# Performance work log

Measured on AMD Instinct MI355X. Metric: run time of the kernel, lower is better.

## Reference

```python
import jax, jax.numpy as jnp
import numpy as np


def setup_inputs() -> dict:
    key = jax.random.key(0)
    ks = jax.random.split(key, 6)
    B, C, W, H = 8, 512, 64, 64
    return {
        "x": jax.random.normal(ks[0], (B, C, W, H), dtype=jnp.float32),
        "proj_query": jax.random.normal(ks[1], (C, W, H), dtype=jnp.float32),
        "key_w": jax.random.normal(ks[2], (C, C), dtype=jnp.float32) * 0.02,
        "key_b": jax.random.normal(ks[3], (C,), dtype=jnp.float32) * 0.02,
        "value_w": jax.random.normal(ks[4], (C, C), dtype=jnp.float32) * 0.02,
        "value_b": jax.random.normal(ks[5], (C,), dtype=jnp.float32) * 0.02,
        "gamma": jnp.ones((1,), dtype=jnp.float32),
    }


def reference(x, proj_query, key_w, key_b, value_w, value_b, gamma):
    B, C, W, H = x.shape
    N = W * H
    # fixed memory query: (C, N); torch builds B x N x C via permute
    q = proj_query.reshape(C, N)
    # 1x1 convs == per-pixel channel matmuls
    k = jnp.einsum('oc,bchw->bohw', key_w, x) + key_b[None, :, None, None]
    v = jnp.einsum('oc,bchw->bohw', value_w, x) + value_b[None, :, None, None]
    k = k.reshape(B, C, N)
    v = v.reshape(B, C, N)
    # energy = bmm(key [B,C,N], query^T [N,C]) -> B x C x C (channel attention)
    energy = jnp.einsum('bcn,dn->bcd', k, q)
    attention = jax.nn.softmax(energy, axis=-1)
    # out = bmm(attention^T [B,C,C], value [B,C,N]) -> B x C x N
    out = jnp.einsum('bdc,bdn->bcn', attention, v)
    out = out.reshape(B, C, W, H)
    return gamma * out + x
```

## Files before the change

### kernel.cpp

```cpp
#include <hip/hip_runtime.h>

typedef unsigned short u16;
typedef unsigned int u32;
typedef unsigned long long u64;
typedef _Float16 f16x8 __attribute__((ext_vector_type(8)));
typedef float f32x4 __attribute__((ext_vector_type(4)));

__device__ __forceinline__ u16 f2h(float f) {
  union { _Float16 h; u16 u; } c; c.h = (_Float16)f; return c.u;
}
__device__ __forceinline__ float h2f(u16 v) {
  union { u16 u; _Float16 h; } c; c.u = v; return (float)c.h;
}

__device__ __forceinline__ f32x4 mfma16(f16x8 a, f16x8 b, f32x4 c) {
  return __builtin_amdgcn_mfma_f32_16x16x32_f16(a, b, c, 0, 0, 0);
}

__device__ __forceinline__ void ld8f(const float* s, u16* o) {
  float4 a = *(const float4*)s;
  float4 b = *(const float4*)(s + 4);
  o[0] = f2h(a.x); o[1] = f2h(a.y); o[2] = f2h(a.z); o[3] = f2h(a.w);
  o[4] = f2h(b.x); o[5] = f2h(b.y); o[6] = f2h(b.z); o[7] = f2h(b.w);
}

__device__ __forceinline__ void cvt8(float4 a, float4 b, u16* o) {
  o[0] = f2h(a.x); o[1] = f2h(a.y); o[2] = f2h(a.z); o[3] = f2h(a.w);
  o[4] = f2h(b.x); o[5] = f2h(b.y); o[6] = f2h(b.z); o[7] = f2h(b.w);
}

__device__ __forceinline__ void addcvt8(float4 a0, float4 a1, float4 c0, float4 c1, u16* o) {
  o[0] = f2h(a0.x + c0.x); o[1] = f2h(a0.y + c0.y); o[2] = f2h(a0.z + c0.z); o[3] = f2h(a0.w + c0.w);
  o[4] = f2h(a1.x + c1.x); o[5] = f2h(a1.y + c1.y); o[6] = f2h(a1.z + c1.z); o[7] = f2h(a1.w + c1.w);
}

__device__ __forceinline__ void glds16(const u16* g, u16* l) {
  __builtin_amdgcn_global_load_lds(
      reinterpret_cast<const __attribute__((address_space(1))) u32*>(reinterpret_cast<u64>(g)),
      reinterpret_cast<__attribute__((address_space(3))) u32*>(reinterpret_cast<u64>(l)),
      16, 0, 0);
}

template<int TM, int TN, int WM, int WN, int DEPTH>
__device__ __forceinline__ void gemm_core(const u16* __restrict__ A, int lda,
                                          const u16* __restrict__ B, int ldb,
                                          int ksteps, u16* sA, u16* sB, f32x4 acc[TM][TN]) {
  constexpr int NT = WM * WN * 64;
  constexpr int BM = WM * TM * 16, BN = WN * TN * 16;
  constexpr int TILEA = BM * 32, TILEB = BN * 32;
  constexpr int APF = (BM * 4) / NT, BPF = (BN * 4) / NT;
  constexpr int VPI = APF + BPF;
  constexpr int PF = DEPTH - 2;
  static_assert(PF == 1 || PF == 2, "");
  static_assert(APF >= 1 && BPF >= 1, "");

  const int t = threadIdx.x;
  const int lane = t & 63, wave = t >> 6;
  const int wm = wave / WN, wn = wave % WN;
  const int m16 = lane & 15, q4 = lane >> 4;

  int aoff[APF], asl[APF];
#pragma unroll
  for (int p = 0; p < APF; ++p) {
    int s = p * NT + t, row = s >> 2;
    int kc = (s & 3) ^ ((row >> 1) & 3);
    aoff[p] = row * lda + kc * 8;
    asl[p] = (p * NT + (wave << 6)) * 8;
  }
  int boff[BPF], bsl[BPF];
#pragma unroll
  for (int p = 0; p < BPF; ++p) {
    int s = p * NT + t, row = s >> 2;
    int kc = (s & 3) ^ ((row >> 1) & 3);
    boff[p] = row * ldb + kc * 8;
    bsl[p] = (p * NT + (wave << 6)) * 8;
  }

  int aro[TM], bro[TN];
#pragma unroll
  for (int i = 0; i < TM; ++i) {
    int row = wm * TM * 16 + i * 16 + m16;
    aro[i] = row * 32 + ((q4 ^ ((row >> 1) & 3)) << 3);
  }
#pragma unroll
  for (int j = 0; j < TN; ++j) {
    int row = wn * TN * 16 + j * 16 + m16;
    bro[j] = row * 32 + ((q4 ^ ((row >> 1) & 3)) << 3);
  }

#pragma unroll
  for (int j = 0; j < PF; ++j) {
    const u16* Aj = A + j * 32;
    u16* aS = sA + j * TILEA;
#pragma unroll
    for (int p = 0; p < APF; ++p) glds16(Aj + aoff[p], aS + asl[p]);
    const u16* Bj = B + j * 32;
    u16* bS = sB + j * TILEB;
#pragma unroll
    for (int p = 0; p < BPF; ++p) glds16(Bj + boff[p], bS + bsl[p]);
  }

  int cur = 0, stg = PF;
#pragma unroll 1
  for (int kt = 0; kt < ksteps; ++kt) {
    if (kt + PF < ksteps) {
      const u16* An = A + (size_t)(kt + PF) * 32;
      u16* aS = sA + stg * TILEA;
#pragma unroll
      for (int p = 0; p < APF; ++p) glds16(An + aoff[p], aS + asl[p]);
      const u16* Bn = B + (size_t)(kt + PF) * 32;
      u16* bS = sB + stg * TILEB;
#pragma unroll
      for (int p = 0; p < BPF; ++p) glds16(Bn + boff[p], bS + bsl[p]);
    }
    if (PF == 2 && kt + 2 < ksteps)
      asm volatile("s_waitcnt vmcnt(%0)" :: "n"(2 * VPI) : "memory");
    else if (kt + 1 < ksteps)
      asm volatile("s_waitcnt vmcnt(%0)" :: "n"(VPI) : "memory");
    else
      asm volatile("s_waitcnt vmcnt(0)" ::: "memory");
    __builtin_amdgcn_s_barrier();
    __builtin_amdgcn_sched_barrier(0);

    const u16* aR = sA + cur * TILEA;
    const u16* bR = sB + cur * TILEB;
    f16x8 af[TM], bv[TN];
#pragma unroll
    for (int i = 0; i < TM; ++i) af[i] = *(const f16x8*)&aR[aro[i]];
#pragma unroll
    for (int j = 0; j < TN; ++j) bv[j] = *(const f16x8*)&bR[bro[j]];
#pragma unroll
    for (int i = 0; i < TM; ++i)
#pragma unroll
      for (int j = 0; j < TN; ++j)
        acc[i][j] = mfma16(af[i], bv[j], acc[i][j]);

    cur = (cur + 1 == DEPTH) ? 0 : cur + 1;
    stg = (stg + 1 == DEPTH) ? 0 : stg + 1;
  }
}

__global__ __launch_bounds__(256) void prep_all_kernel(const float* __restrict__ x,
                                                       u16* __restrict__ xh, u16* __restrict__ xhT,
                                                       const float* __restrict__ q, u16* __restrict__ qh,
                                                       float* __restrict__ qs,
                                                       const float* __restrict__ vw, u16* __restrict__ vwT,
                                                       const float* __restrict__ kw, u16* __restrict__ kwh,
                                                       float* __restrict__ beta) {
  __shared__ __align__(16) u32 TS[64 * 257];
  int blk = blockIdx.x, t = threadIdx.x;
  if (blk < 512) {
    int nt = blk & 63, b = blk >> 6;
    int s = t & 31;
    int c = (t >> 5) * 8;
    const float* xbase = x + ((size_t)b * 512 + 2 * s) * 4096 + nt * 64 + c;

    float4 ca0 = *(const float4*)xbase;
    float4 ca1 = *(const float4*)(xbase + 4);
    float4 cb0 = *(const float4*)(xbase + 4096);
    float4 cb1 = *(const float4*)(xbase + 4100);

#pragma unroll 1
    for (int ot = 0; ot < 8; ++ot) {
      float4 na0, na1, nb0, nb1;
      if (ot < 7) {
        const float* np = xbase + (size_t)(ot + 1) * 64 * 4096;
        na0 = *(const float4*)np;
        na1 = *(const float4*)(np + 4);
        nb0 = *(const float4*)(np + 4096);
        nb1 = *(const float4*)(np + 4100);
      }
      u16 r0[8], r1[8];
      cvt8(ca0, ca1, r0);
      cvt8(cb0, cb1, r1);

      u16* xq = xh + ((size_t)b * 512 + ot * 64 + 2 * s) * 4096 + nt * 64 + c;
      *(int4*)xq = *(int4*)r0;
      *(int4*)(xq + 4096) = *(int4*)r1;

#pragma unroll
      for (int e = 0; e < 8; ++e)
        TS[(c + e) * 257 + ot * 32 + s] = (u32)r0[e] | ((u32)r1[e] << 16);

      ca0 = na0; ca1 = na1; cb0 = nb0; cb1 = nb1;
    }
    __syncthreads();

    int n = t & 63, w = t >> 6;
    const u32* Trow = TS + n * 257 + w * 64;
    u16* xo = xhT + ((size_t)b * 4096 + nt * 64 + n) * 512 + w * 128;
#pragma unroll
    for (int i = 0; i < 16; ++i) {
      u32 vv[4];
      vv[0] = Trow[4 * i]; vv[1] = Trow[4 * i + 1];
      vv[2] = Trow[4 * i + 2]; vv[3] = Trow[4 * i + 3];
      *(int4*)(xo + 8 * i) = *(int4*)vv;
    }
  } else if (blk < 1024) {
    int row = blk - 512;
    float s = 0.f;
#pragma unroll
    for (int p = 0; p < 2; ++p) {
      size_t i = (size_t)row * 4096 + p * 2048 + t * 8;
      u16 o[8];
      ld8f(q + i, o);
#pragma unroll
      for (int e = 0; e < 8; ++e) s += h2f(o[e]);
      *(int4*)&qh[i] = *(int4*)o;
    }
    for (int off = 32; off; off >>= 1) s += __shfl_xor(s, off);
    __shared__ float wsum[4];
    if ((t & 63) == 0) wsum[t >> 6] = s;
    __syncthreads();
    if (t == 0) qs[row] = wsum[0] + wsum[1] + wsum[2] + wsum[3];
  } else if (blk < 1280) {
    int bi = blk - 1024;
    u16* sT = (u16*)TS;
    int bx = bi & 15, by = bi >> 4;
#pragma unroll
    for (int p = 0; p < 4; ++p) {
      int idx = p * 256 + t; int r = idx >> 5, c = idx & 31;
      sT[r * 33 + c] = f2h(vw[(size_t)(by * 32 + r) * 512 + bx * 32 + c]);
    }
    __syncthreads();
#pragma unroll
    for (int p = 0; p < 4; ++p) {
      int idx = p * 256 + t; int r = idx >> 5, c = idx & 31;
      vwT[(size_t)(bx * 32 + r) * 512 + by * 32 + c] = sT[c * 33 + r];
    }
  } else if (blk < 1408) {
    size_t i = ((size_t)(blk - 1280) * 256 + t) * 8;
    u16 o[8];
    ld8f(kw + i, o);
    *(int4*)&kwh[i] = *(int4*)o;
  } else {
    for (int i = t; i < 4096; i += 256) beta[i] = 0.f;
  }
}

__global__ __launch_bounds__(256) void sgemm_kernel(const u16* __restrict__ qh, const u16* __restrict__ xh,
                                                    float* __restrict__ Sp0, float* __restrict__ Sp1) {
  __shared__ __align__(16) u16 sA[4 * 128 * 32], sB[4 * 128 * 32];
  int rt = blockIdx.x, jt = blockIdx.y, ks = blockIdx.z;
  int b = rt >> 2, o0 = (rt & 3) * 128;
  f32x4 acc[4][4];
#pragma unroll
  for (int i = 0; i < 4; ++i)
#pragma unroll
    for (int j = 0; j < 4; ++j) acc[i][j] = (f32x4){0.f, 0.f, 0.f, 0.f};
  gemm_core<4, 4, 2, 2, 4>(qh + (size_t)jt * 128 * 4096 + (size_t)ks * 2048, 4096,
                           xh + ((size_t)b * 512 + o0) * 4096 + (size_t)ks * 2048, 4096,
                           64, sA, sB, acc);

  const int t = threadIdx.x, lane = t & 63, wave = t >> 6;
  const int wm = wave >> 1, wn = wave & 1, m16 = lane & 15, q4 = lane >> 4;
  float* Sp = ks ? Sp1 : Sp0;
  float* Ob = Sp + (size_t)b * 262144;
#pragma unroll
  for (int i = 0; i < 4; ++i)
#pragma unroll
    for (int j = 0; j < 4; ++j)
#pragma unroll
      for (int r2 = 0; r2 < 4; ++r2) {
        int y = jt * 128 + wm * 64 + i * 16 + q4 * 4 + r2;
        int o = o0 + wn * 64 + j * 16 + m16;
        Ob[(size_t)y * 512 + o] = acc[i][j][r2];
      }
}

__global__ __launch_bounds__(256) void egemm_kernel(const u16* __restrict__ kwh,
                                                    const float* __restrict__ Sp0,
                                                    const float* __restrict__ Sp1,
                                                    float* __restrict__ E) {
  __shared__ __align__(16) u16 sA[16 * 2048];
  __shared__ __align__(16) u16 sB[3 * 2048];
  int xt = blockIdx.x >> 3, yt = blockIdx.x & 7, b = blockIdx.y;
  const int t = threadIdx.x, lane = t & 63, wave = t >> 6;
  const int wm = wave >> 1, wn = wave & 1, m16 = lane & 15, q4 = lane >> 4;

  {
    int row = t >> 2;
    int kc = (t & 3) ^ ((row >> 1) & 3);
    const u16* Abase = kwh + (size_t)(xt * 64 + row) * 512 + kc * 8;
    u16* adst = sA + (t & 192) * 8;
#pragma unroll
    for (int k2 = 0; k2 < 16; ++k2)
      glds16(Abase + k2 * 32, adst + k2 * 2048);
  }

  int srow = t >> 2;
  int skc = (t & 3) ^ ((srow >> 1) & 3);
  const float* b0 = Sp0 + (size_t)b * 262144 + (size_t)(yt * 64 + srow) * 512 + skc * 8;
  const float* b1 = Sp1 + (size_t)b * 262144 + (size_t)(yt * 64 + srow) * 512 + skc * 8;

  float4 pa0, pa1, pa2, pa3, pb0, pb1, pb2, pb3;
  pa0 = *(const float4*)(b0);      pa1 = *(const float4*)(b0 + 4);
  pa2 = *(const float4*)(b1);      pa3 = *(const float4*)(b1 + 4);
  pb0 = *(const float4*)(b0 + 32); pb1 = *(const float4*)(b0 + 36);
  pb2 = *(const float4*)(b1 + 32); pb3 = *(const float4*)(b1 + 36);
  {
    u16 h[8];
    addcvt8(pa0, pa1, pa2, pa3, h);
    *(int4*)&sB[t * 8] = *(int4*)h;
  }
  asm volatile("s_waitcnt vmcnt(0) lgkmcnt(0)" ::: "memory");
  __builtin_amdgcn_s_barrier();

  int aro[2], bro[2];
#pragma unroll
  for (int i = 0; i < 2; ++i) {
    int row = wm * 32 + i * 16 + m16;
    aro[i] = row * 32 + ((q4 ^ ((row >> 1) & 3)) << 3);
  }
#pragma unroll
  for (int j = 0; j < 2; ++j) {
    int row = wn * 32 + j * 16 + m16;
    bro[j] = row * 32 + ((q4 ^ ((row >> 1) & 3)) << 3);
  }

  f32x4 acc[2][2];
#pragma unroll
  for (int i = 0; i < 2; ++i)
#pragma unroll
    for (int j = 0; j < 2; ++j) acc[i][j] = (f32x4){0.f, 0.f, 0.f, 0.f};

#pragma unroll 2
  for (int kt = 0; kt < 16; ++kt) {
    if (kt + 2 < 16) {
      const float* s0 = b0 + (kt + 2) * 32;
      const float* s1 = b1 + (kt + 2) * 32;
      if (kt & 1) {
        pb0 = *(const float4*)s0; pb1 = *(const float4*)(s0 + 4);
        pb2 = *(const float4*)s1; pb3 = *(const float4*)(s1 + 4);
      } else {
        pa0 = *(const float4*)s0; pa1 = *(const float4*)(s0 + 4);
        pa2 = *(const float4*)s1; pa3 = *(const float4*)(s1 + 4);
      }
    }
    if (kt + 1 < 16) {
      u16 h[8];
      if (kt & 1) addcvt8(pa0, pa1, pa2, pa3, h);
      else        addcvt8(pb0, pb1, pb2, pb3, h);
      *(int4*)&sB[((kt + 1) % 3) * 2048 + t * 8] = *(int4*)h;
    }
    asm volatile("s_waitcnt lgkmcnt(0)" ::: "memory");
    __builtin_amdgcn_s_barrier();
    __builtin_amdgcn_sched_barrier(0);

    const u16* aT = sA + kt * 2048;
    const u16* bT = sB + (kt % 3) * 2048;
    f16x8 af[2], bv[2];
#pragma unroll
    for (int i = 0; i < 2; ++i) af[i] = *(const f16x8*)&aT[aro[i]];
#pragma unroll
    for (int j = 0; j < 2; ++j) bv[j] = *(const f16x8*)&bT[bro[j]];
#pragma unroll
    for (int i = 0; i < 2; ++i)
#pragma unroll
      for (int j = 0; j < 2; ++j)
        acc[i][j] = mfma16(af[i], bv[j], acc[i][j]);
  }

  float* O = E + ((size_t)b * 512 + xt * 64) * 512 + yt * 64;
#pragma unroll
  for (int i = 0; i < 2; ++i)
#pragma unroll
    for (int j = 0; j < 2; ++j)
#pragma unroll
      for (int r2 = 0; r2 < 4; ++r2) {
        int row = wm * 32 + i * 16 + q4 * 4 + r2;
        int col = wn * 32 + j * 16 + m16;
        O[(size_t)row * 512 + col] = acc[i][j][r2];
      }
}

__global__ __launch_bounds__(256) void softmax_kernel(const float* __restrict__ E, const float* __restrict__ qs,
                                                      const float* __restrict__ kb, const float* __restrict__ vb,
                                                      u16* __restrict__ attT, float* __restrict__ beta) {
  __shared__ float sE[16 * 516];
  __shared__ float sM[16], sS[16];
  int i0 = blockIdx.x * 16, b = blockIdx.y, t = threadIdx.x;
  const float* Eb = E + ((size_t)b * 512 + i0) * 512;
  for (int ch = 0; ch < 32; ++ch) {
    int idx = ch * 256 + t;
    int row = idx >> 9, col = idx & 511;
    sE[row * 516 + col] = Eb[(size_t)row * 512 + col] + kb[i0 + row] * qs[col];
  }
  __syncthreads();
  {
    int row = t >> 4, sub = t & 15;
    float mx = -1e30f;
    for (int ii = 0; ii < 32; ++ii) mx = fmaxf(mx, sE[row * 516 + sub + ii * 16]);
    for (int off = 8; off; off >>= 1) mx = fmaxf(mx, __shfl_xor(mx, off));
    float sm = 0.f;
    for (int ii = 0; ii < 32; ++ii) sm += __expf(sE[row * 516 + sub + ii * 16] - mx);
    for (int off = 8; off; off >>= 1) sm += __shfl_xor(sm, off);
    if (sub == 0) { sM[row] = mx; sS[row] = 1.f / sm; }
  }
  __syncthreads();
  float vbr = vb[i0 + (t & 15)];
  u16* Ob = attT + (size_t)b * 262144;
  for (int ch = 0; ch < 32; ++ch) {
    int idx = ch * 256 + t;
    int r = idx & 15, j = idx >> 4;
    float a = __expf(sE[r * 516 + j] - sM[r]) * sS[r];
    Ob[(size_t)j * 512 + i0 + r] = f2h(a);
    float part = a * vbr;
    for (int off = 8; off; off >>= 1) part += __shfl_xor(part, off);
    if (r == 0) atomicAdd(&beta[b * 512 + j], part);
  }
}

__global__ __launch_bounds__(256) void wgemm_kernel(const u16* __restrict__ attT, const u16* __restrict__ vwT,
                                                    u16* __restrict__ W) {
  __shared__ __align__(16) u16 sA[4 * 64 * 32], sB[4 * 64 * 32];
  int ct = blockIdx.x >> 3, ot = blockIdx.x & 7, b = blockIdx.y;
  f32x4 acc[2][2];
#pragma unroll
  for (int i = 0; i < 2; ++i)
#pragma unroll
    for (int j = 0; j < 2; ++j) acc[i][j] = (f32x4){0.f, 0.f, 0.f, 0.f};
  gemm_core<2, 2, 2, 2, 4>(attT + (size_t)b * 262144 + (size_t)ct * 64 * 512, 512,
                           vwT + (size_t)ot * 64 * 512, 512, 16, sA, sB, acc);

  const int t = threadIdx.x, lane = t & 63, wave = t >> 6;
  const int wm = wave >> 1, wn = wave & 1, m16 = lane & 15, q4 = lane >> 4;
  u16* O = W + (size_t)b * 262144 + (size_t)(ct * 64) * 512 + ot * 64;
#pragma unroll
  for (int i = 0; i < 2; ++i)
#pragma unroll
    for (int j = 0; j < 2; ++j)
#pragma unroll
      for (int r2 = 0; r2 < 4; ++r2) {
        int row = wm * 32 + i * 16 + q4 * 4 + r2;
        int col = wn * 32 + j * 16 + m16;
        O[(size_t)row * 512 + col] = f2h(acc[i][j][r2]);
      }
}

__global__ __launch_bounds__(256) void outgemm_kernel(const u16* __restrict__ W, const u16* __restrict__ xhT,
                                                      const u16* __restrict__ xh, const float* __restrict__ beta,
                                                      const float* __restrict__ gm, float* __restrict__ out) {
  __shared__ __align__(16) u16 sA[4 * 128 * 32], sB[4 * 128 * 32];
  int nt = blockIdx.x, ct = blockIdx.y, b = blockIdx.z;
  f32x4 acc[4][4];
#pragma unroll
  for (int i = 0; i < 4; ++i)
#pragma unroll
    for (int j = 0; j < 4; ++j) acc[i][j] = (f32x4){0.f, 0.f, 0.f, 0.f};
  gemm_core<4, 4, 2, 2, 4>(W + (size_t)b * 262144 + (size_t)ct * 128 * 512, 512,
                           xhT + (size_t)b * 2097152 + (size_t)nt * 128 * 512, 512, 16, sA, sB, acc);

  const int t = threadIdx.x, lane = t & 63, wave = t >> 6;
  const int wm = wave >> 1, wn = wave & 1, m16 = lane & 15, q4 = lane >> 4;
  float g = gm[0];
#pragma unroll
  for (int i = 0; i < 4; ++i)
#pragma unroll
    for (int j = 0; j < 4; ++j)
#pragma unroll
      for (int r2 = 0; r2 < 4; ++r2) {
        int c = ct * 128 + wm * 64 + i * 16 + q4 * 4 + r2;
        int n = nt * 128 + wn * 64 + j * 16 + m16;
        size_t idx = (size_t)b * 2097152 + (size_t)c * 4096 + n;
        out[idx] = g * (acc[i][j][r2] + beta[b * 512 + c]) + h2f(xh[idx]);
      }
}

extern "C" void kernel_launch(void* const* d_in, const int* in_sizes, int n_in,
                              void* d_out, int out_size, void* d_ws, size_t ws_size,
                              hipStream_t stream) {
  const float* x  = (const float*)d_in[0];
  const float* pq = (const float*)d_in[1];
  const float* kw = (const float*)d_in[2];
  const float* kb = (const float*)d_in[3];
  const float* vw = (const float*)d_in[4];
  const float* vb = (const float*)d_in[5];
  const float* gm = (const float*)d_in[6];
  float* out = (float*)d_out;

  char* ws = (char*)d_ws;
  u16*   xh   = (u16*)(ws);
  u16*   qh   = (u16*)(ws + (32ull << 20));
  float* E    = (float*)(ws + (32ull << 20));
  u16*   W    = (u16*)(ws + (36ull << 20));
  float* Sp0  = (float*)(ws + (40ull << 20));
  u16*   attT = (u16*)(ws + (48ull << 20));
  u16*   kwh  = (u16*)(ws + (52ull << 20));
  u16*   vwT  = (u16*)(ws + (52ull << 20) + 524288);
  char*  sm   = ws + (53ull << 20);
  float* qs   = (float*)(sm);
  float* beta = (float*)(sm + 4096);
  u16*   xhT  = (u16*)(ws + (54ull << 20));
  float* Sp1  = (float*)(ws + (86ull << 20));

  prep_all_kernel<<<dim3(1409), 256, 0, stream>>>(x, xh, xhT, pq, qh, qs, vw, vwT, kw, kwh, beta);
  sgemm_kernel<<<dim3(32, 4, 2), 256, 0, stream>>>(qh, xh, Sp0, Sp1);
  egemm_kernel<<<dim3(64, 8), 256, 0, stream>>>(kwh, Sp0, Sp1, E);
  softmax_kernel<<<dim3(32, 8), 256, 0, stream>>>(E, qs, kb, vb, attT, beta);
  wgemm_kernel<<<dim3(64, 8), 256, 0, stream>>>(attT, vwT, W);
  outgemm_kernel<<<dim3(32, 4, 8), 256, 0, stream>>>(W, xhT, xh, beta, gm, out);
}
```

Baseline: 240.0 us.

## Drop transposed x copy; read row-major x in out GEMM via in-register transpose

The prep kernel no longer builds a transposed fp16 copy of x (xhT). It now only converts x to fp16 with a simple elementwise pass. The output GEMM gets a new core (gemm_nnb) that loads the B operand straight from the N-contiguous xh layout, interleaves pairs of k rows into swizzled LDS, and double/triple-buffers the A tiles loaded via global_load_lds. This removes a 32MB write plus the LDS transpose in prep. The cost is register-staged B loads and scattered 4-byte LDS stores inside the GEMM loop.

New measurement: 220.7 us. 8.0% less time.

```diff
diff --git a/kernel.cpp b/kernel.cpp
--- a/kernel.cpp
+++ b/kernel.cpp
@@ -20,11 +20,6 @@
 __device__ __forceinline__ void ld8f(const float* s, u16* o) {
   float4 a = *(const float4*)s;
   float4 b = *(const float4*)(s + 4);
-  o[0] = f2h(a.x); o[1] = f2h(a.y); o[2] = f2h(a.z); o[3] = f2h(a.w);
-  o[4] = f2h(b.x); o[5] = f2h(b.y); o[6] = f2h(b.z); o[7] = f2h(b.w);
-}
-
-__device__ __forceinline__ void cvt8(float4 a, float4 b, u16* o) {
   o[0] = f2h(a.x); o[1] = f2h(a.y); o[2] = f2h(a.z); o[3] = f2h(a.w);
   o[4] = f2h(b.x); o[5] = f2h(b.y); o[6] = f2h(b.z); o[7] = f2h(b.w);
 }
@@ -140,64 +135,126 @@
   }
 }
 
+__device__ __forceinline__ void gemm_nnb(const u16* __restrict__ A, int lda,
+                                         const u16* __restrict__ B, int ldb,
+                                         int ksteps, u16* sA, u16* sB, f32x4 acc[4][4]) {
+  const int t = threadIdx.x;
+  const int lane = t & 63, wave = t >> 6;
+  const int wm = wave >> 1, wn = wave & 1;
+  const int m16 = lane & 15, q4 = lane >> 4;
+  constexpr int TILE = 128 * 32;
+
+  int aoff[2], asl[2];
+#pragma unroll
+  for (int p = 0; p < 2; ++p) {
+    int s = p * 256 + t, row = s >> 2;
+    int kc = (s & 3) ^ ((row >> 1) & 3);
+    aoff[p] = row * lda + kc * 8;
+    asl[p] = (p * 256 + (wave << 6)) * 8;
+  }
+  int aro[4];
+#pragma unroll
+  for (int i = 0; i < 4; ++i) {
+    int row = wm * 64 + i * 16 + m16;
+    aro[i] = row * 32 + ((q4 ^ ((row >> 1) & 3)) << 3);
+  }
+
+  const int kk = (t >> 4) * 2;
+  const int nn = (t & 15) * 8;
+  int bwo[8];
+#pragma unroll
+  for (int e = 0; e < 8; ++e) {
+    int n = nn + e;
+    int cc = (kk >> 3) ^ ((n >> 1) & 3) ^ ((n >> 3) & 3);
+    bwo[e] = n * 32 + (cc << 3) + (kk & 7);
+  }
+  int bro[4];
+#pragma unroll
+  for (int j = 0; j < 4; ++j) {
+    int n = wn * 64 + j * 16 + m16;
+    int cc = q4 ^ ((n >> 1) & 3) ^ ((n >> 3) & 3);
+    bro[j] = n * 32 + (cc << 3);
+  }
+
+  u16 *aR = sA, *aS = sA + TILE, *aT = sA + 2 * TILE;
+  u16 *bR = sB, *bS = sB + TILE;
+
+  int4 nb0, nb1;
+  {
+    const u16* src = B + (size_t)kk * ldb + nn;
+    nb0 = *(const int4*)src;
+    nb1 = *(const int4*)(src + ldb);
+    __builtin_amdgcn_sched_barrier(0);
+  }
+  glds16(A + aoff[0], aR + asl[0]);
+  glds16(A + aoff[1], aR + asl[1]);
+  {
+    union { int4 v; u16 h[8]; } u0, u1; u0.v = nb0; u1.v = nb1;
+#pragma unroll
+    for (int e = 0; e < 8; ++e)
+      *(u32*)&bR[bwo[e]] = (u32)u0.h[e] | ((u32)u1.h[e] << 16);
+  }
+
+#pragma unroll 1
+  for (int kt = 0; kt < ksteps; ++kt) {
+    const bool more = kt + 1 < ksteps;
+    if (more) {
+      const u16* src = B + ((size_t)(kt + 1) * 32 + kk) * ldb + nn;
+      nb0 = *(const int4*)src;
+      nb1 = *(const int4*)(src + ldb);
+      __builtin_amdgcn_sched_barrier(0);
+      const u16* An = A + (kt + 1) * 32;
+      glds16(An + aoff[0], aS + asl[0]);
+      glds16(An + aoff[1], aS + asl[1]);
+      asm volatile("s_waitcnt vmcnt(4) lgkmcnt(0)" ::: "memory");
+    } else {
+      asm volatile("s_waitcnt vmcnt(0) lgkmcnt(0)" ::: "memory");
+    }
+    __builtin_amdgcn_s_barrier();
+    __builtin_amdgcn_sched_barrier(0);
+
+    f16x8 af[4], bv[4];
+#pragma unroll
+    for (int i = 0; i < 4; ++i) af[i] = *(const f16x8*)&aR[aro[i]];
+#pragma unroll
+    for (int j = 0; j < 4; ++j) bv[j] = *(const f16x8*)&bR[bro[j]];
+#pragma unroll
+    for (int i = 0; i < 4; ++i)
+#pragma unroll
+      for (int j = 0; j < 4; ++j)
+        acc[i][j] = mfma16(af[i], bv[j], acc[i][j]);
+
+    if (more) {
+      union { int4 v; u16 h[8]; } u0, u1; u0.v = nb0; u1.v = nb1;
+#pragma unroll
+      for (int e = 0; e < 8; ++e)
+        *(u32*)&bS[bwo[e]] = (u32)u0.h[e] | ((u32)u1.h[e] << 16);
+    }
+    { u16* x2 = aR; aR = aS; aS = aT; aT = x2; }
+    { u16* x2 = bR; bR = bS; bS = x2; }
+  }
+}
+
 __global__ __launch_bounds__(256) void prep_all_kernel(const float* __restrict__ x,
-                                                       u16* __restrict__ xh, u16* __restrict__ xhT,
+                                                       u16* __restrict__ xh,
                                                        const float* __restrict__ q, u16* __restrict__ qh,
                                                        float* __restrict__ qs,
                                                        const float* __restrict__ vw, u16* __restrict__ vwT,
                                                        const float* __restrict__ kw, u16* __restrict__ kwh,
                                                        float* __restrict__ beta) {
-  __shared__ __align__(16) u32 TS[64 * 257];
+  __shared__ u16 sT[32 * 33];
   int blk = blockIdx.x, t = threadIdx.x;
-  if (blk < 512) {
-    int nt = blk & 63, b = blk >> 6;
-    int s = t & 31;
-    int c = (t >> 5) * 8;
-    const float* xbase = x + ((size_t)b * 512 + 2 * s) * 4096 + nt * 64 + c;
-
-    float4 ca0 = *(const float4*)xbase;
-    float4 ca1 = *(const float4*)(xbase + 4);
-    float4 cb0 = *(const float4*)(xbase + 4096);
-    float4 cb1 = *(const float4*)(xbase + 4100);
-
-#pragma unroll 1
-    for (int ot = 0; ot < 8; ++ot) {
-      float4 na0, na1, nb0, nb1;
-      if (ot < 7) {
-        const float* np = xbase + (size_t)(ot + 1) * 64 * 4096;
-        na0 = *(const float4*)np;
-        na1 = *(const float4*)(np + 4);
-        nb0 = *(const float4*)(np + 4096);
-        nb1 = *(const float4*)(np + 4100);
-      }
-      u16 r0[8], r1[8];
-      cvt8(ca0, ca1, r0);
-      cvt8(cb0, cb1, r1);
-
-      u16* xq = xh + ((size_t)b * 512 + ot * 64 + 2 * s) * 4096 + nt * 64 + c;
-      *(int4*)xq = *(int4*)r0;
-      *(int4*)(xq + 4096) = *(int4*)r1;
-
-#pragma unroll
-      for (int e = 0; e < 8; ++e)
-        TS[(c + e) * 257 + ot * 32 + s] = (u32)r0[e] | ((u32)r1[e] << 16);
-
-      ca0 = na0; ca1 = na1; cb0 = nb0; cb1 = nb1;
-    }
-    __syncthreads();
-
-    int n = t & 63, w = t >> 6;
-    const u32* Trow = TS + n * 257 + w * 64;
-    u16* xo = xhT + ((size_t)b * 4096 + nt * 64 + n) * 512 + w * 128;
-#pragma unroll
-    for (int i = 0; i < 16; ++i) {
-      u32 vv[4];
-      vv[0] = Trow[4 * i]; vv[1] = Trow[4 * i + 1];
-      vv[2] = Trow[4 * i + 2]; vv[3] = Trow[4 * i + 3];
-      *(int4*)(xo + 8 * i) = *(int4*)vv;
-    }
-  } else if (blk < 1024) {
-    int row = blk - 512;
+  if (blk < 2048) {
+    size_t base = (size_t)blk * 8192;
+#pragma unroll
+    for (int p = 0; p < 4; ++p) {
+      size_t i = base + p * 2048 + t * 8;
+      u16 o[8];
+      ld8f(x + i, o);
+      *(int4*)&xh[i] = *(int4*)o;
+    }
+  } else if (blk < 2560) {
+    int row = blk - 2048;
     float s = 0.f;
 #pragma unroll
     for (int p = 0; p < 2; ++p) {
@@ -213,9 +270,8 @@
     if ((t & 63) == 0) wsum[t >> 6] = s;
     __syncthreads();
     if (t == 0) qs[row] = wsum[0] + wsum[1] + wsum[2] + wsum[3];
-  } else if (blk < 1280) {
-    int bi = blk - 1024;
-    u16* sT = (u16*)TS;
+  } else if (blk < 2816) {
+    int bi = blk - 2560;
     int bx = bi & 15, by = bi >> 4;
 #pragma unroll
     for (int p = 0; p < 4; ++p) {
@@ -228,8 +284,8 @@
       int idx = p * 256 + t; int r = idx >> 5, c = idx & 31;
       vwT[(size_t)(bx * 32 + r) * 512 + by * 32 + c] = sT[c * 33 + r];
     }
-  } else if (blk < 1408) {
-    size_t i = ((size_t)(blk - 1280) * 256 + t) * 8;
+  } else if (blk < 2944) {
+    size_t i = ((size_t)(blk - 2816) * 256 + t) * 8;
     u16 o[8];
     ld8f(kw + i, o);
     *(int4*)&kwh[i] = *(int4*)o;
@@ -438,18 +494,18 @@
       }
 }
 
-__global__ __launch_bounds__(256) void outgemm_kernel(const u16* __restrict__ W, const u16* __restrict__ xhT,
-                                                      const u16* __restrict__ xh, const float* __restrict__ beta,
+__global__ __launch_bounds__(256) void outgemm_kernel(const u16* __restrict__ W, const u16* __restrict__ xh,
+                                                      const float* __restrict__ beta,
                                                       const float* __restrict__ gm, float* __restrict__ out) {
-  __shared__ __align__(16) u16 sA[4 * 128 * 32], sB[4 * 128 * 32];
+  __shared__ __align__(16) u16 sA[3 * 128 * 32], sB[2 * 128 * 32];
   int nt = blockIdx.x, ct = blockIdx.y, b = blockIdx.z;
   f32x4 acc[4][4];
 #pragma unroll
   for (int i = 0; i < 4; ++i)
 #pragma unroll
     for (int j = 0; j < 4; ++j) acc[i][j] = (f32x4){0.f, 0.f, 0.f, 0.f};
-  gemm_core<4, 4, 2, 2, 4>(W + (size_t)b * 262144 + (size_t)ct * 128 * 512, 512,
-                           xhT + (size_t)b * 2097152 + (size_t)nt * 128 * 512, 512, 16, sA, sB, acc);
+  gemm_nnb(W + (size_t)b * 262144 + (size_t)ct * 128 * 512, 512,
+           xh + (size_t)b * 2097152 + nt * 128, 4096, 16, sA, sB, acc);
 
   const int t = threadIdx.x, lane = t & 63, wave = t >> 6;
   const int wm = wave >> 1, wn = wave & 1, m16 = lane & 15, q4 = lane >> 4;
@@ -491,13 +547,12 @@
   char*  sm   = ws + (53ull << 20);
   float* qs   = (float*)(sm);
   float* beta = (float*)(sm + 4096);
-  u16*   xhT  = (u16*)(ws + (54ull << 20));
   float* Sp1  = (float*)(ws + (86ull << 20));
 
-  prep_all_kernel<<<dim3(1409), 256, 0, stream>>>(x, xh, xhT, pq, qh, qs, vw, vwT, kw, kwh, beta);
+  prep_all_kernel<<<dim3(2945), 256, 0, stream>>>(x, xh, pq, qh, qs, vw, vwT, kw, kwh, beta);
   sgemm_kernel<<<dim3(32, 4, 2), 256, 0, stream>>>(qh, xh, Sp0, Sp1);
   egemm_kernel<<<dim3(64, 8), 256, 0, stream>>>(kwh, Sp0, Sp1, E);
   softmax_kernel<<<dim3(32, 8), 256, 0, stream>>>(E, qs, kb, vb, attT, beta);
   wgemm_kernel<<<dim3(64, 8), 256, 0, stream>>>(attT, vwT, W);
-  outgemm_kernel<<<dim3(32, 4, 8), 256, 0, stream>>>(W, xhT, xh, beta, gm, out);
-}
+  outgemm_kernel<<<dim3(32, 4, 8), 256, 0, stream>>>(W, xh, beta, gm, out);
+}
```
